# Kernel tuning notes

Hardware: AMD Instinct MI355X
Metric: run time of the kernel (lower is better)

The kernel has to match this reference:

```python
import jax, jax.numpy as jnp
import numpy as np

T_B = 0.9   # GIoU threshold
T_C = 0.2   # KL threshold
EPS = 1e-9
LOGIT_EPS = 1e-6

def box_cxcywh_to_xyxy(b):
    cx, cy, w, h = b[..., 0], b[..., 1], b[..., 2], b[..., 3]
    return jnp.stack([cx - 0.5 * w, cy - 0.5 * h, cx + 0.5 * w, cy + 0.5 * h], axis=-1)

def pairwise_giou(boxes):
    # boxes: [n, 4] xyxy -> [n, n] generalized IoU
    area = (boxes[:, 2] - boxes[:, 0]) * (boxes[:, 3] - boxes[:, 1])  # [n]
    lt = jnp.maximum(boxes[:, None, :2], boxes[None, :, :2])   # [n, n, 2]
    rb = jnp.minimum(boxes[:, None, 2:], boxes[None, :, 2:])
    wh = jnp.clip(rb - lt, 0.0)
    inter = wh[..., 0] * wh[..., 1]                              # [n, n]
    union = area[:, None] + area[None, :] - inter
    iou = inter / (union + EPS)
    # smallest enclosing box
    lt_e = jnp.minimum(boxes[:, None, :2], boxes[None, :, :2])
    rb_e = jnp.maximum(boxes[:, None, 2:], boxes[None, :, 2:])
    wh_e = jnp.clip(rb_e - lt_e, 0.0)
    area_e = wh_e[..., 0] * wh_e[..., 1]
    return iou - (area_e - union) / (area_e + EPS)

def build_aggregation_mask(bboxes_i, logits_i):
    # bboxes_i: [n_q, 4] cxcywh; logits_i: [n_q, C]. All non-differentiable.
    n_q = bboxes_i.shape[0]
    giou = pairwise_giou(box_cxcywh_to_xyxy(bboxes_i))           # [n_q, n_q]
    iou_gt = giou > T_B
    # pairwise KL between per-query (normalized) class distributions
    p = jax.nn.sigmoid(logits_i)
    q = p / (jnp.sum(p, axis=-1, keepdims=True) + EPS)           # [n_q, C]
    logq = jnp.log(q + EPS)
    self_ent = jnp.sum(q * logq, axis=-1)                        # [n_q]
    kl = self_ent[:, None] - q @ logq.T                          # kl[i,j] = KL(q_i || q_j)
    kl_lt = kl < T_C
    mask = iou_gt & kl_lt
    mask = mask | mask.T                                         # symmetrize
    # transitive closure via repeated boolean squaring (log2(n_q)+1 iters suffice)
    adj = mask.astype(jnp.float32)
    n_iters = int(np.ceil(np.log2(n_q))) + 1
    for _ in range(n_iters):
        adj = ((adj + adj @ adj) > 0).astype(jnp.float32)
    # dedup clusters: keep row i only if i is the smallest member of its cluster
    adj_bool = adj > 0
    first_member = jnp.argmax(adj_bool, axis=1)                  # first True per row
    keep = (first_member == jnp.arange(n_q)).astype(jnp.float32)
    return adj * keep[:, None]                                   # [n_q, n_q] float32

def aggregate_one(bboxes_i, logits_i):
    agg_mask = jax.lax.stop_gradient(
        build_aggregation_mask(jax.lax.stop_gradient(bboxes_i),
                               jax.lax.stop_gradient(logits_i)))
    denom = jnp.maximum(jnp.sum(agg_mask, axis=-1, keepdims=True), 1.0)  # [n_q, 1]
    agg_bboxes = (agg_mask @ bboxes_i) / denom                   # [n_q, 4]
    prob = jax.nn.sigmoid(logits_i)
    agg_prob = (agg_mask @ prob) / denom                         # [n_q, C]
    agg_prob = jnp.clip(agg_prob, LOGIT_EPS, 1.0 - LOGIT_EPS)
    agg_logits = jnp.log(agg_prob) - jnp.log1p(-agg_prob)        # logit with eps
    return agg_bboxes, agg_logits

def setup_inputs() -> dict:
    key = jax.random.key(0)
    k1, k2 = jax.random.split(key)
    bboxes = jax.random.uniform(k1, (64, 900, 4), dtype=jnp.float32)
    logits = jax.random.normal(k2, (64, 900, 91), dtype=jnp.float32)
    return {"bboxes": bboxes, "logits": logits}

def reference(bboxes, logits):
    return jax.vmap(aggregate_one)(bboxes, logits)
```

## Files before the change

### kernel.cpp

```cpp
#include <hip/hip_runtime.h>
#include <math.h>

#define NB 64
#define NQ 900
#define NC 91
#define TB_THR 0.9f
#define TC_THR 0.2f
#define EPSF 1e-9f
#define LGEPS 1e-6f

#define TPB 256
#define TT 120
#define SUB 60
#define TPAIRS 36
#define EDGE_BLOCKS (NB * TPAIRS)
#define INIT_BLOCKS 225
#define SP_BLOCKS 225
#define OUT4_BLOCKS 5344

__device__ __forceinline__ int uf_find(int* p, int x) {
    volatile int* vp = (volatile int*)p;
    int px = vp[x];
    while (px != x) { x = px; px = vp[x]; }
    return x;
}

__device__ void uf_unite(int* p, int a, int b) {
    while (true) {
        a = uf_find(p, a);
        b = uf_find(p, b);
        if (a == b) return;
        int hi = a > b ? a : b;
        int lo = a ^ b ^ hi;
        if (atomicCAS(&p[hi], hi, lo) == hi) return;
        a = hi; b = lo;
    }
}

__device__ __forceinline__ void do_pair(float4 R, float ai, float4 B, float aj,
                                        bool val, int gi, int gj,
                                        int* __restrict__ ncand,
                                        int2* __restrict__ cand, int cap) {
    float ltx = fmaxf(R.x, B.x), lty = fmaxf(R.y, B.y);
    float rbx = fminf(R.z, B.z), rby = fminf(R.w, B.w);
    float w = fmaxf(rbx - ltx, 0.f), h = fmaxf(rby - lty, 0.f);
    float inter = w * h;
    float uni = ai + aj - inter;
    if (val && inter > TB_THR * (uni + EPSF)) {
        float ex = fmaxf(fmaxf(R.z, B.z) - fminf(R.x, B.x), 0.f);
        float ey = fmaxf(fmaxf(R.w, B.w) - fminf(R.y, B.y), 0.f);
        float ae = ex * ey;
        float iou = inter / (uni + EPSF);
        float giou = iou - (ae - uni) / (ae + EPSF);
        if (giou > TB_THR) {
            int pos = atomicAdd(ncand, 1);
            if (pos < cap) cand[pos] = make_int2(gi, gj);
        }
    }
}

__global__ __launch_bounds__(TPB)
void k_edges_init(const float* __restrict__ bboxes,
                  int* __restrict__ parent, int* __restrict__ cnt,
                  int* __restrict__ ncand, int2* __restrict__ cand, int cap) {
    __shared__ float4 jb[TT];
    __shared__ float  ja[TT];
    int bid = blockIdx.x;
    if (bid >= EDGE_BLOCKS) {
        int idx = (bid - EDGE_BLOCKS) * TPB + threadIdx.x;
        if (idx < NB * NQ) { parent[idx] = idx; cnt[idx] = 0; }
        return;
    }
    int b = bid / TPAIRS, tp = bid % TPAIRS;
    int tj = (int)((sqrtf(8.f * tp + 1.f) - 1.f) * 0.5f);
    while ((tj + 1) * (tj + 2) / 2 <= tp) ++tj;
    while (tj * (tj + 1) / 2 > tp) --tj;
    int ti = tp - tj * (tj + 1) / 2;
    int i0 = ti * TT, j0 = tj * TT;
    const float4* bb = (const float4*)(bboxes + (size_t)b * NQ * 4);

    int jend = NQ - j0; if (jend > TT) jend = TT;
    for (int k = threadIdx.x; k < jend; k += TPB) {
        float4 v = bb[j0 + k];
        float4 e = make_float4(v.x - 0.5f * v.z, v.y - 0.5f * v.w,
                               v.x + 0.5f * v.z, v.y + 0.5f * v.w);
        jb[k] = e;
        ja[k] = (e.z - e.x) * (e.w - e.y);
    }
    __syncthreads();

    int lane = threadIdx.x & 63;
    int wv   = threadIdx.x >> 6;
    bool lv  = lane < SUB;
    int iA = i0 + (lv ? lane : 0);
    int iB = iA + SUB;
    bool vB = lv && (iB < NQ);

    float4 a4 = bb[iA];
    float4 RA = make_float4(a4.x - 0.5f * a4.z, a4.y - 0.5f * a4.w,
                            a4.x + 0.5f * a4.z, a4.y + 0.5f * a4.w);
    float aA = (RA.z - RA.x) * (RA.w - RA.y);
    float4 b4 = bb[vB ? iB : iA];
    float4 RB = make_float4(b4.x - 0.5f * b4.z, b4.y - 0.5f * b4.w,
                            b4.x + 0.5f * b4.z, b4.y + 0.5f * b4.w);
    float aB = (RB.z - RB.x) * (RB.w - RB.y);

    int gbase = b * NQ;
    int jlo = wv * 30, jhi = jlo + 30; if (jhi > jend) jhi = jend;
    for (int jj = jlo; jj < jhi; ++jj) {
        int j = j0 + jj;
        float4 B = jb[jj];
        float aj = ja[jj];
        do_pair(RA, aA, B, aj, lv && (iA < j), gbase + iA, gbase + j, ncand, cand, cap);
        do_pair(RB, aB, B, aj, vB && (iB < j), gbase + iB, gbase + j, ncand, cand, cap);
    }
}

__global__ __launch_bounds__(TPB)
void k_kl(const float* __restrict__ logits, const int* __restrict__ ncand,
          const int2* __restrict__ cand, int cap, int* __restrict__ parent) {
    int n = *ncand; if (n > cap) n = cap;
    int wid  = (int)((blockIdx.x * TPB + threadIdx.x) >> 6);
    int lane = threadIdx.x & 63;
    int nw   = (int)((gridDim.x * TPB) >> 6);
    for (int m = wid; m < n; m += nw) {
        int2 pr = cand[m];
        const float* li = logits + (size_t)pr.x * NC;
        const float* lj = logits + (size_t)pr.y * NC;
        int c1 = lane + 64;
        bool h1 = (c1 < NC);
        float pi0 = 1.f / (1.f + expf(-li[lane]));
        float pj0 = 1.f / (1.f + expf(-lj[lane]));
        float pi1 = h1 ? 1.f / (1.f + expf(-li[c1])) : 0.f;
        float pj1 = h1 ? 1.f / (1.f + expf(-lj[c1])) : 0.f;
        float si = pi0 + pi1, sj = pj0 + pj1;
        for (int o = 32; o; o >>= 1) { si += __shfl_xor(si, o); sj += __shfl_xor(sj, o); }
        float di = si + EPSF, dj = sj + EPSF;
        float qi0 = pi0 / di, qi1 = pi1 / di, qj0 = pj0 / dj, qj1 = pj1 / dj;
        float lqi0 = logf(qi0 + EPSF), lqj0 = logf(qj0 + EPSF);
        float lqi1 = h1 ? logf(qi1 + EPSF) : 0.f;
        float lqj1 = h1 ? logf(qj1 + EPSF) : 0.f;
        float ei  = qi0 * lqi0 + (h1 ? qi1 * lqi1 : 0.f);
        float ej  = qj0 * lqj0 + (h1 ? qj1 * lqj1 : 0.f);
        float dij = qi0 * lqj0 + (h1 ? qi1 * lqj1 : 0.f);
        float dji = qj0 * lqi0 + (h1 ? qj1 * lqi1 : 0.f);
        for (int o = 32; o; o >>= 1) {
            ei  += __shfl_xor(ei, o);  ej  += __shfl_xor(ej, o);
            dij += __shfl_xor(dij, o); dji += __shfl_xor(dji, o);
        }
        bool edge = ((ei - dij) < TC_THR) || ((ej - dji) < TC_THR);
        if (edge && lane == 0) uf_unite(parent, pr.x, pr.y);
    }
}

__global__ void k_flatten(const int* __restrict__ parent,
                          int* __restrict__ label, int* __restrict__ cnt) {
    int idx = blockIdx.x * blockDim.x + threadIdx.x;
    if (idx >= NB * NQ) return;
    int r = idx;
    while (parent[r] != r) r = parent[r];
    label[idx] = r;
    atomicAdd(&cnt[r], 1);
}

__global__ __launch_bounds__(TPB)
void k_out(const float* __restrict__ bboxes, const float* __restrict__ logits,
           const int* __restrict__ label, const int* __restrict__ cnt,
           float* __restrict__ out) {
    const long long NBB  = (long long)NB * NQ * 4;
    const long long NTOT = NBB + (long long)NB * NQ * NC;
    const float LO = logf(LGEPS) - log1pf(-LGEPS);
    const float HI = logf(1.f - LGEPS) - log1pf(-(1.f - LGEPS));
    int bid = blockIdx.x;
    if (bid < SP_BLOCKS) {
        int wv   = bid * 4 + (threadIdx.x >> 6);
        int lane = threadIdx.x & 63;
        int r0   = wv * 64;
        int r    = r0 + lane;
        bool flag = (label[r] == r) && (cnt[r] > 1);
        unsigned long long mask = __ballot(flag);
        while (mask) {
            int bit = __ffsll((long long)mask) - 1; mask &= mask - 1;
            int R = r0 + bit;
            int b = R / NQ;
            int base = b * NQ;
            float a0 = 0.f, a1 = 0.f, ab = 0.f;
            for (int it = 0; it < 15; ++it) {
                int row = it * 64 + lane;
                bool mem = (row < NQ) && (label[base + row] == R);
                unsigned long long mm = __ballot(mem);
                while (mm) {
                    int mb = __ffsll((long long)mm) - 1; mm &= mm - 1;
                    int g = base + it * 64 + mb;
                    const float* lg = logits + (size_t)g * NC;
                    a0 += 1.f / (1.f + expf(-lg[lane]));
                    if (lane + 64 < NC) a1 += 1.f / (1.f + expf(-lg[lane + 64]));
                    if (lane < 4)       ab += bboxes[(size_t)g * 4 + lane];
                }
            }
            float d = fmaxf((float)cnt[R], 1.f);
            if (lane < 4) out[(size_t)R * 4 + lane] = ab / d;
            {
                float v = fminf(fmaxf(a0 / d, LGEPS), 1.f - LGEPS);
                out[NBB + (size_t)R * NC + lane] = logf(v) - log1pf(-v);
            }
            if (lane + 64 < NC) {
                float v = fminf(fmaxf(a1 / d, LGEPS), 1.f - LGEPS);
                out[NBB + (size_t)R * NC + lane + 64] = logf(v) - log1pf(-v);
            }
        }
        return;
    }
    long long q4 = (long long)(bid - SP_BLOCKS) * TPB + threadIdx.x;
    if (q4 >= NTOT / 4) return;
    long long idx = q4 * 4;
    if (idx < NBB) {
        int g = (int)(idx >> 2);
        int r = label[g];
        float4 o;
        if (r != g) o = make_float4(0.f, 0.f, 0.f, 0.f);
        else if (cnt[g] == 1) o = ((const float4*)bboxes)[g];
        else return;
        ((float4*)out)[q4] = o;
        return;
    }
    long long t = idx - NBB;
    int g0 = (int)(t / NC), g3 = (int)((t + 3) / NC);
    if (g0 == g3) {
        int r = label[g0];
        float4 o;
        if (r != g0) o = make_float4(LO, LO, LO, LO);
        else if (cnt[g0] == 1) {
            float4 L = *(const float4*)(logits + t);
            o = make_float4(fminf(fmaxf(L.x, LO), HI), fminf(fmaxf(L.y, LO), HI),
                            fminf(fmaxf(L.z, LO), HI), fminf(fmaxf(L.w, LO), HI));
        } else return;
        ((float4*)out)[q4] = o;
    } else {
#pragma unroll
        for (int e = 0; e < 4; ++e) {
            long long te = t + e;
            int g = (int)(te / NC);
            int r = label[g];
            if (r != g) out[idx + e] = LO;
            else if (cnt[g] == 1) out[idx + e] = fminf(fmaxf(logits[te], LO), HI);
        }
    }
}

extern "C" void kernel_launch(void* const* d_in, const int* in_sizes, int n_in,
                              void* d_out, int out_size, void* d_ws, size_t ws_size,
                              hipStream_t stream) {
    const float* bboxes = (const float*)d_in[0];
    const float* logits = (const float*)d_in[1];
    float* out = (float*)d_out;

    char* ws = (char*)d_ws;
    const int NROWS = NB * NQ;
    int* parent = (int*)(ws);
    int* label  = (int*)(ws + 1 * NROWS * 4);
    int* cnt    = (int*)(ws + 2 * NROWS * 4);
    int* ncand  = (int*)(ws + 3 * NROWS * 4);
    int2* cand  = (int2*)(ws + 3 * NROWS * 4 + 256);
    size_t base = (size_t)(3 * NROWS * 4 + 256);
    long long cap_ll = ws_size > base ? (long long)((ws_size - base) / sizeof(int2)) : 0;
    int cap = (int)(cap_ll > (1 << 20) ? (1 << 20) : cap_ll);

    hipMemsetAsync(ncand, 0, sizeof(int), stream);

    k_edges_init<<<EDGE_BLOCKS + INIT_BLOCKS, TPB, 0, stream>>>(
        bboxes, parent, cnt, ncand, cand, cap);

    k_kl<<<512, TPB, 0, stream>>>(logits, ncand, cand, cap, parent);

    k_flatten<<<INIT_BLOCKS, TPB, 0, stream>>>(parent, label, cnt);

    k_out<<<SP_BLOCKS + OUT4_BLOCKS, TPB, 0, stream>>>(bboxes, logits, label, cnt, out);
}
```

Before: 58.04 us.

## Fuse KL test into GIoU sweep and do union-find in single block

```diff
diff --git a/kernel.cpp b/kernel.cpp
--- a/kernel.cpp
+++ b/kernel.cpp
@@ -15,8 +15,9 @@
 #define TPAIRS 36
 #define EDGE_BLOCKS (NB * TPAIRS)
 #define INIT_BLOCKS 225
-#define SP_BLOCKS 225
 #define OUT4_BLOCKS 5344
+#define SLOT 64
+#define MAXE 4096
 
 __device__ __forceinline__ int uf_find(int* p, int x) {
     volatile int* vp = (volatile int*)p;
@@ -37,96 +38,30 @@
     }
 }
 
-__device__ __forceinline__ void do_pair(float4 R, float ai, float4 B, float aj,
-                                        bool val, int gi, int gj,
-                                        int* __restrict__ ncand,
-                                        int2* __restrict__ cand, int cap) {
+__device__ __forceinline__ bool pair_test(float4 R, float ai, float4 B, float aj) {
     float ltx = fmaxf(R.x, B.x), lty = fmaxf(R.y, B.y);
     float rbx = fminf(R.z, B.z), rby = fminf(R.w, B.w);
     float w = fmaxf(rbx - ltx, 0.f), h = fmaxf(rby - lty, 0.f);
     float inter = w * h;
     float uni = ai + aj - inter;
-    if (val && inter > TB_THR * (uni + EPSF)) {
-        float ex = fmaxf(fmaxf(R.z, B.z) - fminf(R.x, B.x), 0.f);
-        float ey = fmaxf(fmaxf(R.w, B.w) - fminf(R.y, B.y), 0.f);
-        float ae = ex * ey;
-        float iou = inter / (uni + EPSF);
-        float giou = iou - (ae - uni) / (ae + EPSF);
-        if (giou > TB_THR) {
-            int pos = atomicAdd(ncand, 1);
-            if (pos < cap) cand[pos] = make_int2(gi, gj);
-        }
-    }
-}
-
-__global__ __launch_bounds__(TPB)
-void k_edges_init(const float* __restrict__ bboxes,
-                  int* __restrict__ parent, int* __restrict__ cnt,
-                  int* __restrict__ ncand, int2* __restrict__ cand, int cap) {
-    __shared__ float4 jb[TT];
-    __shared__ float  ja[TT];
-    int bid = blockIdx.x;
-    if (bid >= EDGE_BLOCKS) {
-        int idx = (bid - EDGE_BLOCKS) * TPB + threadIdx.x;
-        if (idx < NB * NQ) { parent[idx] = idx; cnt[idx] = 0; }
-        return;
-    }
-    int b = bid / TPAIRS, tp = bid % TPAIRS;
-    int tj = (int)((sqrtf(8.f * tp + 1.f) - 1.f) * 0.5f);
-    while ((tj + 1) * (tj + 2) / 2 <= tp) ++tj;
-    while (tj * (tj + 1) / 2 > tp) --tj;
-    int ti = tp - tj * (tj + 1) / 2;
-    int i0 = ti * TT, j0 = tj * TT;
-    const float4* bb = (const float4*)(bboxes + (size_t)b * NQ * 4);
-
-    int jend = NQ - j0; if (jend > TT) jend = TT;
-    for (int k = threadIdx.x; k < jend; k += TPB) {
-        float4 v = bb[j0 + k];
-        float4 e = make_float4(v.x - 0.5f * v.z, v.y - 0.5f * v.w,
-                               v.x + 0.5f * v.z, v.y + 0.5f * v.w);
-        jb[k] = e;
-        ja[k] = (e.z - e.x) * (e.w - e.y);
-    }
-    __syncthreads();
-
-    int lane = threadIdx.x & 63;
-    int wv   = threadIdx.x >> 6;
-    bool lv  = lane < SUB;
-    int iA = i0 + (lv ? lane : 0);
-    int iB = iA + SUB;
-    bool vB = lv && (iB < NQ);
-
-    float4 a4 = bb[iA];
-    float4 RA = make_float4(a4.x - 0.5f * a4.z, a4.y - 0.5f * a4.w,
-                            a4.x + 0.5f * a4.z, a4.y + 0.5f * a4.w);
-    float aA = (RA.z - RA.x) * (RA.w - RA.y);
-    float4 b4 = bb[vB ? iB : iA];
-    float4 RB = make_float4(b4.x - 0.5f * b4.z, b4.y - 0.5f * b4.w,
-                            b4.x + 0.5f * b4.z, b4.y + 0.5f * b4.w);
-    float aB = (RB.z - RB.x) * (RB.w - RB.y);
-
-    int gbase = b * NQ;
-    int jlo = wv * 30, jhi = jlo + 30; if (jhi > jend) jhi = jend;
-    for (int jj = jlo; jj < jhi; ++jj) {
-        int j = j0 + jj;
-        float4 B = jb[jj];
-        float aj = ja[jj];
-        do_pair(RA, aA, B, aj, lv && (iA < j), gbase + iA, gbase + j, ncand, cand, cap);
-        do_pair(RB, aB, B, aj, vB && (iB < j), gbase + iB, gbase + j, ncand, cand, cap);
-    }
-}
-
-__global__ __launch_bounds__(TPB)
-void k_kl(const float* __restrict__ logits, const int* __restrict__ ncand,
-          const int2* __restrict__ cand, int cap, int* __restrict__ parent) {
-    int n = *ncand; if (n > cap) n = cap;
-    int wid  = (int)((blockIdx.x * TPB + threadIdx.x) >> 6);
-    int lane = threadIdx.x & 63;
-    int nw   = (int)((gridDim.x * TPB) >> 6);
-    for (int m = wid; m < n; m += nw) {
-        int2 pr = cand[m];
-        const float* li = logits + (size_t)pr.x * NC;
-        const float* lj = logits + (size_t)pr.y * NC;
+    if (!(inter > TB_THR * (uni + EPSF))) return false;
+    float ex = fmaxf(fmaxf(R.z, B.z) - fminf(R.x, B.x), 0.f);
+    float ey = fmaxf(fmaxf(R.w, B.w) - fminf(R.y, B.y), 0.f);
+    float ae = ex * ey;
+    float iou = inter / (uni + EPSF);
+    float giou = iou - (ae - uni) / (ae + EPSF);
+    return giou > TB_THR;
+}
+
+__device__ void kl_process(unsigned long long m, int ibase, int j, int gbase,
+                           const float* __restrict__ logits, int lane,
+                           int* lcnt, int2* lbuf) {
+    while (m) {
+        int src = __ffsll((long long)m) - 1; m &= m - 1;
+        int gi = gbase + ibase + src;
+        int gj = gbase + j;
+        const float* li = logits + (size_t)gi * NC;
+        const float* lj = logits + (size_t)gj * NC;
         int c1 = lane + 64;
         bool h1 = (c1 < NC);
         float pi0 = 1.f / (1.f + expf(-li[lane]));
@@ -149,77 +84,167 @@
             dij += __shfl_xor(dij, o); dji += __shfl_xor(dji, o);
         }
         bool edge = ((ei - dij) < TC_THR) || ((ej - dji) < TC_THR);
-        if (edge && lane == 0) uf_unite(parent, pr.x, pr.y);
-    }
-}
-
-__global__ void k_flatten(const int* __restrict__ parent,
-                          int* __restrict__ label, int* __restrict__ cnt) {
-    int idx = blockIdx.x * blockDim.x + threadIdx.x;
-    if (idx >= NB * NQ) return;
-    int r = idx;
-    while (parent[r] != r) r = parent[r];
-    label[idx] = r;
-    atomicAdd(&cnt[r], 1);
+        if (edge && lane == 0) {
+            int pos = atomicAdd(lcnt, 1);
+            if (pos < SLOT) lbuf[pos] = make_int2(gi, gj);
+        }
+    }
+}
+
+__global__ __launch_bounds__(TPB)
+void k_sweep(const float* __restrict__ bboxes, const float* __restrict__ logits,
+             int* __restrict__ parent, int* __restrict__ ovl,
+             int* __restrict__ bcnt, int2* __restrict__ slots) {
+    __shared__ float4 jb[TT];
+    __shared__ float  ja[TT];
+    __shared__ int lcnt;
+    __shared__ int2 lbuf[SLOT];
+    int bid = blockIdx.x;
+    if (bid >= EDGE_BLOCKS) {
+        int idx = (bid - EDGE_BLOCKS) * TPB + threadIdx.x;
+        if (idx < NB * NQ) { parent[idx] = idx; ovl[idx] = 0; }
+        return;
+    }
+    if (threadIdx.x == 0) lcnt = 0;
+    int b = bid / TPAIRS, tp = bid % TPAIRS;
+    int tj = (int)((sqrtf(8.f * tp + 1.f) - 1.f) * 0.5f);
+    while ((tj + 1) * (tj + 2) / 2 <= tp) ++tj;
+    while (tj * (tj + 1) / 2 > tp) --tj;
+    int ti = tp - tj * (tj + 1) / 2;
+    int i0 = ti * TT, j0 = tj * TT;
+    const float4* bb = (const float4*)(bboxes + (size_t)b * NQ * 4);
+
+    int jend = NQ - j0; if (jend > TT) jend = TT;
+    for (int k = threadIdx.x; k < jend; k += TPB) {
+        float4 v = bb[j0 + k];
+        float4 e = make_float4(v.x - 0.5f * v.z, v.y - 0.5f * v.w,
+                               v.x + 0.5f * v.z, v.y + 0.5f * v.w);
+        jb[k] = e;
+        ja[k] = (e.z - e.x) * (e.w - e.y);
+    }
+    __syncthreads();
+
+    int lane = threadIdx.x & 63;
+    int wv   = threadIdx.x >> 6;
+    bool lv  = lane < SUB;
+    int iA = i0 + (lv ? lane : 0);
+    int iB = iA + SUB;
+    bool vB = lv && (iB < NQ);
+
+    float4 a4 = bb[iA];
+    float4 RA = make_float4(a4.x - 0.5f * a4.z, a4.y - 0.5f * a4.w,
+                            a4.x + 0.5f * a4.z, a4.y + 0.5f * a4.w);
+    float aA = (RA.z - RA.x) * (RA.w - RA.y);
+    float4 b4 = bb[vB ? iB : iA];
+    float4 RB = make_float4(b4.x - 0.5f * b4.z, b4.y - 0.5f * b4.w,
+                            b4.x + 0.5f * b4.z, b4.y + 0.5f * b4.w);
+    float aB = (RB.z - RB.x) * (RB.w - RB.y);
+
+    int gbase = b * NQ;
+    int jlo = wv * 30, jhi = jlo + 30; if (jhi > jend) jhi = jend;
+    for (int jj = jlo; jj < jhi; ++jj) {
+        int j = j0 + jj;
+        float4 B = jb[jj];
+        float aj = ja[jj];
+        bool fA = lv && (iA < j) && pair_test(RA, aA, B, aj);
+        bool fB = vB && (iB < j) && pair_test(RB, aB, B, aj);
+        unsigned long long mA = __ballot(fA);
+        unsigned long long mB = __ballot(fB);
+        if (mA | mB) {
+            kl_process(mA, i0, j, gbase, logits, lane, &lcnt, lbuf);
+            kl_process(mB, i0 + SUB, j, gbase, logits, lane, &lcnt, lbuf);
+        }
+    }
+    __syncthreads();
+    int n = lcnt < SLOT ? lcnt : SLOT;
+    if (threadIdx.x == 0) bcnt[bid] = n;
+    for (int k = threadIdx.x; k < n; k += TPB) slots[bid * SLOT + k] = lbuf[k];
+}
+
+__global__ __launch_bounds__(1024)
+void k_union(const float* __restrict__ bboxes, const float* __restrict__ logits,
+             int* __restrict__ parent, int* __restrict__ ovl,
+             const int* __restrict__ bcnt, const int2* __restrict__ slots,
+             float* __restrict__ out) {
+    __shared__ int nedge, nroots;
+    __shared__ int2 edges[MAXE];
+    __shared__ int roots[256];
+    int tid = threadIdx.x;
+    if (tid == 0) { nedge = 0; nroots = 0; }
+    __syncthreads();
+    for (int blk = tid; blk < EDGE_BLOCKS; blk += 1024) {
+        int c = bcnt[blk];
+        for (int k = 0; k < c; ++k) {
+            int pos = atomicAdd(&nedge, 1);
+            if (pos < MAXE) edges[pos] = slots[blk * SLOT + k];
+        }
+    }
+    __syncthreads();
+    int ne = nedge < MAXE ? nedge : MAXE;
+    for (int e = tid; e < ne; e += 1024) uf_unite(parent, edges[e].x, edges[e].y);
+    __threadfence();
+    __syncthreads();
+    for (int e = tid; e < ne; e += 1024) {
+        for (int s = 0; s < 2; ++s) {
+            int v = s ? edges[e].y : edges[e].x;
+            if (atomicCAS(&ovl[v], 0, 1) == 0) {
+                int r = uf_find(parent, v);
+                ovl[v] = r + 1;
+                if (r == v) { int p = atomicAdd(&nroots, 1); if (p < 256) roots[p] = r; }
+            }
+        }
+    }
+    __threadfence();
+    __syncthreads();
+    int nr = nroots < 256 ? nroots : 256;
+    int wv = tid >> 6, lane = tid & 63;
+    const long long NBB = (long long)NB * NQ * 4;
+    for (int ri = wv; ri < nr; ri += 16) {
+        int R = roots[ri];
+        int b = R / NQ, base = b * NQ;
+        float a0 = 0.f, a1 = 0.f, ab = 0.f;
+        int cm = 0;
+        for (int it = 0; it < 15; ++it) {
+            int row = it * 64 + lane;
+            bool mem = (row < NQ) && (ovl[base + row] == R + 1);
+            unsigned long long mm = __ballot(mem);
+            cm += __popcll(mm);
+            while (mm) {
+                int mb = __ffsll((long long)mm) - 1; mm &= mm - 1;
+                int g = base + it * 64 + mb;
+                const float* lg = logits + (size_t)g * NC;
+                a0 += 1.f / (1.f + expf(-lg[lane]));
+                if (lane + 64 < NC) a1 += 1.f / (1.f + expf(-lg[lane + 64]));
+                if (lane < 4)       ab += bboxes[(size_t)g * 4 + lane];
+            }
+        }
+        float d = (float)cm;
+        if (lane < 4) out[(size_t)R * 4 + lane] = ab / d;
+        float v0 = fminf(fmaxf(a0 / d, LGEPS), 1.f - LGEPS);
+        out[NBB + (size_t)R * NC + lane] = logf(v0) - log1pf(-v0);
+        if (lane + 64 < NC) {
+            float v1 = fminf(fmaxf(a1 / d, LGEPS), 1.f - LGEPS);
+            out[NBB + (size_t)R * NC + lane + 64] = logf(v1) - log1pf(-v1);
+        }
+    }
 }
 
 __global__ __launch_bounds__(TPB)
 void k_out(const float* __restrict__ bboxes, const float* __restrict__ logits,
-           const int* __restrict__ label, const int* __restrict__ cnt,
-           float* __restrict__ out) {
+           const int* __restrict__ ovl, float* __restrict__ out) {
     const long long NBB  = (long long)NB * NQ * 4;
     const long long NTOT = NBB + (long long)NB * NQ * NC;
     const float LO = logf(LGEPS) - log1pf(-LGEPS);
     const float HI = logf(1.f - LGEPS) - log1pf(-(1.f - LGEPS));
-    int bid = blockIdx.x;
-    if (bid < SP_BLOCKS) {
-        int wv   = bid * 4 + (threadIdx.x >> 6);
-        int lane = threadIdx.x & 63;
-        int r0   = wv * 64;
-        int r    = r0 + lane;
-        bool flag = (label[r] == r) && (cnt[r] > 1);
-        unsigned long long mask = __ballot(flag);
-        while (mask) {
-            int bit = __ffsll((long long)mask) - 1; mask &= mask - 1;
-            int R = r0 + bit;
-            int b = R / NQ;
-            int base = b * NQ;
-            float a0 = 0.f, a1 = 0.f, ab = 0.f;
-            for (int it = 0; it < 15; ++it) {
-                int row = it * 64 + lane;
-                bool mem = (row < NQ) && (label[base + row] == R);
-                unsigned long long mm = __ballot(mem);
-                while (mm) {
-                    int mb = __ffsll((long long)mm) - 1; mm &= mm - 1;
-                    int g = base + it * 64 + mb;
-                    const float* lg = logits + (size_t)g * NC;
-                    a0 += 1.f / (1.f + expf(-lg[lane]));
-                    if (lane + 64 < NC) a1 += 1.f / (1.f + expf(-lg[lane + 64]));
-                    if (lane < 4)       ab += bboxes[(size_t)g * 4 + lane];
-                }
-            }
-            float d = fmaxf((float)cnt[R], 1.f);
-            if (lane < 4) out[(size_t)R * 4 + lane] = ab / d;
-            {
-                float v = fminf(fmaxf(a0 / d, LGEPS), 1.f - LGEPS);
-                out[NBB + (size_t)R * NC + lane] = logf(v) - log1pf(-v);
-            }
-            if (lane + 64 < NC) {
-                float v = fminf(fmaxf(a1 / d, LGEPS), 1.f - LGEPS);
-                out[NBB + (size_t)R * NC + lane + 64] = logf(v) - log1pf(-v);
-            }
-        }
-        return;
-    }
-    long long q4 = (long long)(bid - SP_BLOCKS) * TPB + threadIdx.x;
+    long long q4 = (long long)blockIdx.x * TPB + threadIdx.x;
     if (q4 >= NTOT / 4) return;
     long long idx = q4 * 4;
     if (idx < NBB) {
         int g = (int)(idx >> 2);
-        int r = label[g];
+        int v = ovl[g];
         float4 o;
-        if (r != g) o = make_float4(0.f, 0.f, 0.f, 0.f);
-        else if (cnt[g] == 1) o = ((const float4*)bboxes)[g];
+        if (v == 0)            o = ((const float4*)bboxes)[g];
+        else if (v - 1 != g)   o = make_float4(0.f, 0.f, 0.f, 0.f);
         else return;
         ((float4*)out)[q4] = o;
         return;
@@ -227,23 +252,23 @@
     long long t = idx - NBB;
     int g0 = (int)(t / NC), g3 = (int)((t + 3) / NC);
     if (g0 == g3) {
-        int r = label[g0];
+        int v = ovl[g0];
         float4 o;
-        if (r != g0) o = make_float4(LO, LO, LO, LO);
-        else if (cnt[g0] == 1) {
+        if (v == 0) {
             float4 L = *(const float4*)(logits + t);
             o = make_float4(fminf(fmaxf(L.x, LO), HI), fminf(fmaxf(L.y, LO), HI),
                             fminf(fmaxf(L.z, LO), HI), fminf(fmaxf(L.w, LO), HI));
-        } else return;
+        } else if (v - 1 != g0) o = make_float4(LO, LO, LO, LO);
+        else return;
         ((float4*)out)[q4] = o;
     } else {
 #pragma unroll
         for (int e = 0; e < 4; ++e) {
             long long te = t + e;
             int g = (int)(te / NC);
-            int r = label[g];
-            if (r != g) out[idx + e] = LO;
-            else if (cnt[g] == 1) out[idx + e] = fminf(fmaxf(logits[te], LO), HI);
+            int v = ovl[g];
+            if (v == 0)          out[idx + e] = fminf(fmaxf(logits[te], LO), HI);
+            else if (v - 1 != g) out[idx + e] = LO;
         }
     }
 }
@@ -257,23 +282,15 @@
 
     char* ws = (char*)d_ws;
     const int NROWS = NB * NQ;
-    int* parent = (int*)(ws);
-    int* label  = (int*)(ws + 1 * NROWS * 4);
-    int* cnt    = (int*)(ws + 2 * NROWS * 4);
-    int* ncand  = (int*)(ws + 3 * NROWS * 4);
-    int2* cand  = (int2*)(ws + 3 * NROWS * 4 + 256);
-    size_t base = (size_t)(3 * NROWS * 4 + 256);
-    long long cap_ll = ws_size > base ? (long long)((ws_size - base) / sizeof(int2)) : 0;
-    int cap = (int)(cap_ll > (1 << 20) ? (1 << 20) : cap_ll);
-
-    hipMemsetAsync(ncand, 0, sizeof(int), stream);
-
-    k_edges_init<<<EDGE_BLOCKS + INIT_BLOCKS, TPB, 0, stream>>>(
-        bboxes, parent, cnt, ncand, cand, cap);
-
-    k_kl<<<512, TPB, 0, stream>>>(logits, ncand, cand, cap, parent);
-
-    k_flatten<<<INIT_BLOCKS, TPB, 0, stream>>>(parent, label, cnt);
-
-    k_out<<<SP_BLOCKS + OUT4_BLOCKS, TPB, 0, stream>>>(bboxes, logits, label, cnt, out);
-}
+    int*  parent = (int*) (ws);
+    int*  ovl    = (int*) (ws + 1 * NROWS * 4);
+    int*  bcnt   = (int*) (ws + 2 * NROWS * 4);
+    int2* slots  = (int2*)(ws + 2 * NROWS * 4 + 16384);
+
+    k_sweep<<<EDGE_BLOCKS + INIT_BLOCKS, TPB, 0, stream>>>(
+        bboxes, logits, parent, ovl, bcnt, slots);
+
+    k_union<<<1, 1024, 0, stream>>>(bboxes, logits, parent, ovl, bcnt, slots, out);
+
+    k_out<<<OUT4_BLOCKS, TPB, 0, stream>>>(bboxes, logits, ovl, out);
+}
```

Result: slower. 110.2 us (+89.8%).
